# Optimization experiments

Hardware: AMD Instinct MI355X
Metric: run time of the kernel (lower is better)

## Reference

```python
import jax, jax.numpy as jnp
import numpy as np

NUM_EXPERTS = 8
CAPACITY = 320  # per-batch per-expert token capacity


def setup_inputs() -> dict:
    key = jax.random.key(0)
    k0, k1, k2, k3 = jax.random.split(key, 4)
    B, S, D, F = 4, 2048, 1024, 4096
    E = NUM_EXPERTS
    hidden_states = jax.random.normal(k0, (B, S, D), dtype=jnp.float32)
    gate_w = jax.random.normal(k1, (E, D), dtype=jnp.float32) * 0.02
    w1 = jax.random.normal(k2, (E, D, F), dtype=jnp.float32) * 0.02
    w2 = jax.random.normal(k3, (E, F, D), dtype=jnp.float32) * 0.02
    return {"hidden_states": hidden_states, "gate_w": gate_w, "w1": w1, "w2": w2}


def reference(hidden_states, gate_w, w1, w2):
    E, C = NUM_EXPERTS, CAPACITY
    B, S, D = hidden_states.shape

    # --- route ---
    router_logits = jnp.einsum('bsd,ed->bse', hidden_states, gate_w)
    router_probs = jax.nn.softmax(router_logits, axis=-1)
    expert_idx = jnp.argmax(router_probs, axis=-1)                      # [B,S]
    onehot = jax.nn.one_hot(expert_idx, E, dtype=jnp.int32)             # [B,S,E]
    priority = jnp.cumsum(onehot, axis=1)                               # [B,S,E]
    router_mask = onehot * (priority <= C)                              # [B,S,E]
    assigned = jnp.sum(router_mask, axis=-1) > 0                        # [B,S]
    # slot within expert buffer; dropped tokens go to overflow slot C
    slot = jnp.where(assigned, jnp.sum(priority * onehot, axis=-1) - 1, C)  # [B,S]
    top_prob = jnp.max(router_probs, axis=-1, keepdims=True)            # [B,S,1]

    # --- dispatch: scatter tokens into [B,E,C+1,D] buffers ---
    def dispatch(x_b, e_b, s_b):
        return jnp.zeros((E, C + 1, D), x_b.dtype).at[e_b, s_b].set(x_b)
    buf = jax.vmap(dispatch)(hidden_states, expert_idx, slot)           # [B,E,C+1,D]

    # --- per-expert FFN as grouped GEMM ---
    h = jax.nn.silu(jnp.einsum('becd,edf->becf', buf, w1))
    y = jnp.einsum('becf,efd->becd', h, w2)                             # [B,E,C+1,D]

    # --- combine: gather expert outputs back to token order ---
    gathered = jax.vmap(lambda y_b, e_b, s_b: y_b[e_b, s_b])(y, expert_idx, slot)  # [B,S,D]
    next_states = jnp.where(assigned[..., None], gathered, hidden_states)
    out = top_prob * next_states

    # argmax of capacity-masked one-hot: dropped tokens -> expert 0
    expert_index = jnp.where(assigned, expert_idx, 0)
    return out, router_logits, expert_index
```

## Files before the change

### kernel.cpp

```cpp
#include <hip/hip_runtime.h>

#define B_  4
#define S_  2048
#define D_  1024
#define F_  4096
#define E_  8
#define C_  320
#define CP_ 384
#define NT_ (B_*S_)
#define G_  (B_*E_)

typedef short bf16x8 __attribute__((ext_vector_type(8)));
typedef float f32x4  __attribute__((ext_vector_type(4)));

using gptr_t = const __attribute__((address_space(1))) void*;
using lptr_t = __attribute__((address_space(3))) void*;

__device__ static inline void gll16(const void* g, void* l) {
    __builtin_amdgcn_global_load_lds((gptr_t)g, (lptr_t)l, 16, 0, 0);
}

__device__ static inline unsigned short f2b(float f) {
    unsigned int u = __float_as_uint(f);
    u += 0x7fffu + ((u >> 16) & 1u);
    return (unsigned short)(u >> 16);
}

__global__ __launch_bounds__(256) void k_convT(const float* __restrict__ in,
                                               unsigned short* __restrict__ out,
                                               int R, int Cc) {
    __shared__ unsigned short ld[64][66];
    int e = blockIdx.z;
    const float* src = in + (size_t)e * R * Cc;
    unsigned short* dst = out + (size_t)e * R * Cc;
    int c0 = blockIdx.x * 64, r0 = blockIdx.y * 64;
    int t = threadIdx.x;

    int rr = t >> 4;
    int cg = t & 15;
#pragma unroll
    for (int p = 0; p < 4; p++) {
        int row = p * 16 + rr;
        float4 v = *(const float4*)(src + (size_t)(r0 + row) * Cc + c0 + cg * 4);
        ld[cg * 4 + 0][row] = f2b(v.x);
        ld[cg * 4 + 1][row] = f2b(v.y);
        ld[cg * 4 + 2][row] = f2b(v.z);
        ld[cg * 4 + 3][row] = f2b(v.w);
    }
    __syncthreads();

    int cc = t >> 3;
    int rg = t & 7;
#pragma unroll
    for (int p = 0; p < 2; p++) {
        int col = p * 32 + cc;
        const unsigned* lp = (const unsigned*)&ld[col][rg * 8];
        uint4 w;
        w.x = lp[0]; w.y = lp[1]; w.z = lp[2]; w.w = lp[3];
        *(uint4*)(dst + (size_t)(c0 + col) * R + r0 + rg * 8) = w;
    }
}

__global__ __launch_bounds__(256) void k_router(const float* __restrict__ hs,
                                                const float* __restrict__ gw,
                                                float* __restrict__ logits,
                                                int* __restrict__ eidx,
                                                float* __restrict__ tp) {
    int tok  = (int)((blockIdx.x * 256 + threadIdx.x) >> 6);
    int lane = threadIdx.x & 63;
    const float* x = hs + (size_t)tok * D_;
    double acc[E_];
#pragma unroll
    for (int e = 0; e < E_; e++) acc[e] = 0.0;
    for (int i = 0; i < 16; i++) {
        float xv = x[lane + 64 * i];
#pragma unroll
        for (int e = 0; e < E_; e++)
            acc[e] += (double)xv * (double)gw[e * D_ + lane + 64 * i];
    }
#pragma unroll
    for (int e = 0; e < E_; e++) {
#pragma unroll
        for (int off = 32; off > 0; off >>= 1)
            acc[e] += __shfl_xor(acc[e], off, 64);
    }
    if (lane == 0) {
        float l[E_];
        float mx = -1e30f; int am = 0;
#pragma unroll
        for (int e = 0; e < E_; e++) {
            l[e] = (float)acc[e];
            if (l[e] > mx) { mx = l[e]; am = e; }
        }
        float se = 0.f;
#pragma unroll
        for (int e = 0; e < E_; e++) se += __expf(l[e] - mx);
        tp[tok]   = 1.0f / se;
        eidx[tok] = am;
#pragma unroll
        for (int e = 0; e < E_; e++) logits[(size_t)tok * E_ + e] = l[e];
    }
}

__global__ __launch_bounds__(256) void k_scan(const int* __restrict__ eidx,
                                              int* __restrict__ slot,
                                              int* __restrict__ tok_list,
                                              int* __restrict__ counts,
                                              float* __restrict__ eif) {
    int b = blockIdx.x;
    __shared__ int cCnt[32][E_];
    __shared__ int cBase[32][E_];
    int t = threadIdx.x, wv = t >> 6, lane = t & 63;
    const int* eb = eidx + b * S_;
    for (int c = wv; c < 32; c += 4) {
        int e = eb[c * 64 + lane];
#pragma unroll
        for (int x = 0; x < E_; x++) {
            unsigned long long m = __ballot(e == x);
            if (lane == 0) cCnt[c][x] = __popcll(m);
        }
    }
    __syncthreads();
    if (t < E_) {
        int s = 0;
        for (int c = 0; c < 32; c++) { cBase[c][t] = s; s += cCnt[c][t]; }
        counts[b * E_ + t] = s;
    }
    __syncthreads();
    for (int c = wv; c < 32; c += 4) {
        int s_tok = c * 64 + lane;
        int e = eb[s_tok];
        unsigned long long lowmask = (1ull << lane) - 1ull;
        int rank = 0;
#pragma unroll
        for (int x = 0; x < E_; x++) {
            unsigned long long m = __ballot(e == x);
            if (x == e) rank = __popcll(m & lowmask);
        }
        int pos = cBase[c][e] + rank;
        int assigned = (pos < C_);
        slot[b * S_ + s_tok] = assigned ? pos : C_;
        if (assigned) tok_list[(b * E_ + e) * C_ + pos] = s_tok;
        eif[b * S_ + s_tok] = assigned ? (float)e : 0.0f;
    }
}

__global__ __launch_bounds__(256) void k_dispatch(const float* __restrict__ hs,
                                                  const int* __restrict__ tok_list,
                                                  const int* __restrict__ counts,
                                                  unsigned short* __restrict__ Xd) {
    int w    = (int)((blockIdx.x * 256 + threadIdx.x) >> 6);
    int lane = threadIdx.x & 63;
    int g = w / CP_, row = w % CP_;
    int b = g >> 3;
    int n = min(counts[g], C_);
    unsigned short* drow = Xd + ((size_t)g * CP_ + row) * D_;
    if (row < n) {
        int ts = tok_list[g * C_ + row];
        const float* src = hs + ((size_t)b * S_ + ts) * D_;
#pragma unroll
        for (int i = 0; i < 2; i++) {
            int c0 = (lane + 64 * i) * 8;
            float4 v0 = *(const float4*)(src + c0);
            float4 v1 = *(const float4*)(src + c0 + 4);
            uint4 pk;
            pk.x = (unsigned)f2b(v0.x) | ((unsigned)f2b(v0.y) << 16);
            pk.y = (unsigned)f2b(v0.z) | ((unsigned)f2b(v0.w) << 16);
            pk.z = (unsigned)f2b(v1.x) | ((unsigned)f2b(v1.y) << 16);
            pk.w = (unsigned)f2b(v1.z) | ((unsigned)f2b(v1.w) << 16);
            *(uint4*)(drow + c0) = pk;
        }
    } else {
        uint4 z = {0u, 0u, 0u, 0u};
#pragma unroll
        for (int i = 0; i < 2; i++)
            *(uint4*)(drow + (lane + 64 * i) * 8) = z;
    }
}

__global__ __launch_bounds__(256) void k_ffn1(const unsigned short* __restrict__ Xd,
                                              const unsigned short* __restrict__ w1t,
                                              const int* __restrict__ counts,
                                              unsigned short* __restrict__ h) {
    int zz = blockIdx.z;
    int g = (zz & 3) * 8 + (zz >> 2);
    int n_tok = min(counts[g], C_);
    int m0 = blockIdx.y * 128;
    if (m0 >= n_tok) return;
    int n0 = blockIdx.x * 128;
    int e = g & 7;

    __shared__ unsigned short As[128 * 32];
    __shared__ unsigned short Bs[128 * 32];
    int t = threadIdx.x, lane = t & 63, wv = t >> 6, wm = wv >> 1, wn = wv & 1;

    const unsigned short* Ap = Xd  + (size_t)g * CP_ * D_ + (size_t)(m0 + (t >> 2)) * D_ + (t & 3) * 8;
    const unsigned short* Bp = w1t + (size_t)e * F_ * D_  + (size_t)(n0 + (t >> 2)) * D_ + (t & 3) * 8;

    f32x4 acc[4][4];
    f32x4 z = {0.f, 0.f, 0.f, 0.f};
#pragma unroll
    for (int i = 0; i < 4; i++)
#pragma unroll
        for (int j = 0; j < 4; j++) acc[i][j] = z;

    int ar = (wm * 64 + (lane & 15)) * 32 + (lane >> 4) * 8;
    int br = (wn * 64 + (lane & 15)) * 32 + (lane >> 4) * 8;

    for (int kt = 0; kt < D_; kt += 32) {
        __syncthreads();
        gll16(Ap,            (char*)As + wv * 1024);
        gll16(Ap + 64 * D_,  (char*)As + 4096 + wv * 1024);
        gll16(Bp,            (char*)Bs + wv * 1024);
        gll16(Bp + 64 * D_,  (char*)Bs + 4096 + wv * 1024);
        Ap += 32; Bp += 32;
        __syncthreads();
        bf16x8 a[4], bq[4];
#pragma unroll
        for (int i = 0; i < 4; i++) a[i]  = *(const bf16x8*)&As[ar + i * 512];
#pragma unroll
        for (int j = 0; j < 4; j++) bq[j] = *(const bf16x8*)&Bs[br + j * 512];
#pragma unroll
        for (int i = 0; i < 4; i++)
#pragma unroll
            for (int j = 0; j < 4; j++)
                acc[i][j] = __builtin_amdgcn_mfma_f32_16x16x32_bf16(a[i], bq[j], acc[i][j], 0, 0, 0);
    }

    unsigned short* hb = h + (size_t)g * CP_ * F_;
    int crow = m0 + wm * 64 + (lane >> 4) * 4;
    int ccol = n0 + wn * 64 + (lane & 15);
#pragma unroll
    for (int i = 0; i < 4; i++)
#pragma unroll
        for (int r = 0; r < 4; r++) {
            int row = crow + i * 16 + r;
#pragma unroll
            for (int j = 0; j < 4; j++) {
                float v = acc[i][j][r];
                v = v / (1.0f + __expf(-v));
                hb[(size_t)row * F_ + ccol + j * 16] = f2b(v);
            }
        }
}

__global__ __launch_bounds__(256) void k_ffn2(const unsigned short* __restrict__ h,
                                              const unsigned short* __restrict__ w2t,
                                              const int* __restrict__ counts,
                                              const int* __restrict__ tok_list,
                                              const float* __restrict__ tp,
                                              float* __restrict__ out) {
    int zz = blockIdx.z;
    int g = (zz & 3) * 8 + (zz >> 2);
    int n_tok = min(counts[g], C_);
    int m0 = blockIdx.y * 128;
    if (m0 >= n_tok) return;
    int n0 = blockIdx.x * 128;
    int b = g >> 3, e = g & 7;

    __shared__ unsigned short As[128 * 32];
    __shared__ unsigned short Bs[128 * 32];
    int t = threadIdx.x, lane = t & 63, wv = t >> 6, wm = wv >> 1, wn = wv & 1;

    const unsigned short* Ap = h   + (size_t)g * CP_ * F_ + (size_t)(m0 + (t >> 2)) * F_ + (t & 3) * 8;
    const unsigned short* Bp = w2t + (size_t)e * D_ * F_  + (size_t)(n0 + (t >> 2)) * F_ + (t & 3) * 8;

    f32x4 acc[4][4];
    f32x4 z = {0.f, 0.f, 0.f, 0.f};
#pragma unroll
    for (int i = 0; i < 4; i++)
#pragma unroll
        for (int j = 0; j < 4; j++) acc[i][j] = z;

    int ar = (wm * 64 + (lane & 15)) * 32 + (lane >> 4) * 8;
    int br = (wn * 64 + (lane & 15)) * 32 + (lane >> 4) * 8;

    for (int kt = 0; kt < F_; kt += 32) {
        __syncthreads();
        gll16(Ap,            (char*)As + wv * 1024);
        gll16(Ap + 64 * F_,  (char*)As + 4096 + wv * 1024);
        gll16(Bp,            (char*)Bs + wv * 1024);
        gll16(Bp + 64 * F_,  (char*)Bs + 4096 + wv * 1024);
        Ap += 32; Bp += 32;
        __syncthreads();
        bf16x8 a[4], bq[4];
#pragma unroll
        for (int i = 0; i < 4; i++) a[i]  = *(const bf16x8*)&As[ar + i * 512];
#pragma unroll
        for (int j = 0; j < 4; j++) bq[j] = *(const bf16x8*)&Bs[br + j * 512];
#pragma unroll
        for (int i = 0; i < 4; i++)
#pragma unroll
            for (int j = 0; j < 4; j++)
                acc[i][j] = __builtin_amdgcn_mfma_f32_16x16x32_bf16(a[i], bq[j], acc[i][j], 0, 0, 0);
    }

    int crow = m0 + wm * 64 + (lane >> 4) * 4;
    int ccol = n0 + wn * 64 + (lane & 15);
#pragma unroll
    for (int i = 0; i < 4; i++)
#pragma unroll
        for (int r = 0; r < 4; r++) {
            int row = crow + i * 16 + r;
            if (row < n_tok) {
                int ts = tok_list[g * C_ + row];
                float sc = tp[b * S_ + ts];
                float* orow = out + ((size_t)b * S_ + ts) * D_ + ccol;
#pragma unroll
                for (int j = 0; j < 4; j++)
                    orow[j * 16] = sc * acc[i][j][r];
            }
        }
}

__global__ __launch_bounds__(256) void k_pass(const float* __restrict__ hs,
                                              const int* __restrict__ slot,
                                              const float* __restrict__ tp,
                                              float* __restrict__ out) {
    int tok  = (int)((blockIdx.x * 256 + threadIdx.x) >> 6);
    int lane = threadIdx.x & 63;
    if (slot[tok] < C_) return;
    float sc = tp[tok];
    const float* src = hs + (size_t)tok * D_;
    float* dst = out + (size_t)tok * D_;
#pragma unroll
    for (int i = 0; i < 4; i++) {
        float4 v = *(const float4*)(src + (lane + 64 * i) * 4);
        v.x *= sc; v.y *= sc; v.z *= sc; v.w *= sc;
        *(float4*)(dst + (lane + 64 * i) * 4) = v;
    }
}

extern "C" void kernel_launch(void* const* d_in, const int* in_sizes, int n_in,
                              void* d_out, int out_size, void* d_ws, size_t ws_size,
                              hipStream_t stream) {
    const float* hs = (const float*)d_in[0];
    const float* gw = (const float*)d_in[1];
    const float* w1 = (const float*)d_in[2];
    const float* w2 = (const float*)d_in[3];

    float* out    = (float*)d_out;
    float* logits = out + (size_t)NT_ * D_;
    float* eif    = logits + (size_t)NT_ * E_;

    char* ws = (char*)d_ws;
    int*            eidx     = (int*)(ws + 0);
    int*            slot     = (int*)(ws + 65536);
    float*          tp       = (float*)(ws + 131072);
    int*            tok_list = (int*)(ws + 196608);
    int*            counts   = (int*)(ws + 262144);
    unsigned short* Xd       = (unsigned short*)(ws + 327680);
    unsigned short* w1t      = (unsigned short*)(ws + 33554432ull);
    unsigned short* w2t      = (unsigned short*)(ws + 100663296ull);
    unsigned short* hbuf     = (unsigned short*)(ws + 167772160ull);

    dim3 blk(256);
    k_convT<<<dim3(F_ / 64, D_ / 64, E_), blk, 0, stream>>>(w1, w1t, D_, F_);
    k_convT<<<dim3(D_ / 64, F_ / 64, E_), blk, 0, stream>>>(w2, w2t, F_, D_);
    k_router<<<dim3(NT_ / 4), blk, 0, stream>>>(hs, gw, logits, eidx, tp);
    k_scan<<<dim3(B_), blk, 0, stream>>>(eidx, slot, tok_list, counts, eif);
    k_dispatch<<<dim3(G_ * CP_ / 4), blk, 0, stream>>>(hs, tok_list, counts, Xd);
    k_ffn1<<<dim3(F_ / 128, CP_ / 128, G_), blk, 0, stream>>>(Xd, w1t, counts, hbuf);
    k_ffn2<<<dim3(D_ / 128, CP_ / 128, G_), blk, 0, stream>>>(hbuf, w2t, counts, tok_list, tp, out);
    k_pass<<<dim3(NT_ / 4), blk, 0, stream>>>(hs, slot, tp, out);
}
```

Before: 599.4 us.

## Merge batches per expert into one grouped GEMM with 256x256 double-buffered tiles

Tokens are now regrouped per expert across all batches into one padded M dimension, using new base offsets and a global token list. Each expert's weights are then streamed once per M-tile rather than once per batch-expert group. The FFN GEMMs use a shared core: 512 threads, 256x256 output tiles, double-buffered LDS filled by direct global-to-LDS loads, an XOR swizzle, and barrier-separated MFMA phases with priority boosts. This adds a small extra launch and uses 128KB of LDS per block. The second GEMM launches only 160 blocks, which may leave CUs idle.

```diff
diff --git a/kernel.cpp b/kernel.cpp
--- a/kernel.cpp
+++ b/kernel.cpp
@@ -6,9 +6,8 @@
 #define F_  4096
 #define E_  8
 #define C_  320
-#define CP_ 384
+#define MPAD_ 1280
 #define NT_ (B_*S_)
-#define G_  (B_*E_)
 
 typedef short bf16x8 __attribute__((ext_vector_type(8)));
 typedef float f32x4  __attribute__((ext_vector_type(4)));
@@ -145,18 +144,38 @@
     }
 }
 
+__global__ void k_base(const int* __restrict__ counts,
+                       int* __restrict__ ebase,
+                       int* __restrict__ nE) {
+    int e = threadIdx.x;
+    if (e < E_) {
+        int s = 0;
+#pragma unroll
+        for (int b = 0; b < B_; b++) {
+            ebase[b * E_ + e] = s;
+            s += min(counts[b * E_ + e], C_);
+        }
+        nE[e] = s;
+    }
+}
+
 __global__ __launch_bounds__(256) void k_dispatch(const float* __restrict__ hs,
-                                                  const int* __restrict__ tok_list,
-                                                  const int* __restrict__ counts,
+                                                  const int* __restrict__ tlB,
+                                                  const int* __restrict__ ebase,
+                                                  const int* __restrict__ nE,
+                                                  int* __restrict__ tlG,
                                                   unsigned short* __restrict__ Xd) {
     int w    = (int)((blockIdx.x * 256 + threadIdx.x) >> 6);
     int lane = threadIdx.x & 63;
-    int g = w / CP_, row = w % CP_;
-    int b = g >> 3;
-    int n = min(counts[g], C_);
-    unsigned short* drow = Xd + ((size_t)g * CP_ + row) * D_;
-    if (row < n) {
-        int ts = tok_list[g * C_ + row];
+    int e = w / MPAD_, r = w - e * MPAD_;
+    unsigned short* drow = Xd + ((size_t)e * MPAD_ + r) * D_;
+    if (r < nE[e]) {
+        int b = 0;
+#pragma unroll
+        for (int bb = 1; bb < B_; bb++) if (r >= ebase[bb * E_ + e]) b = bb;
+        int pos = r - ebase[b * E_ + e];
+        int ts  = tlB[(b * E_ + e) * C_ + pos];
+        if (lane == 0) tlG[e * MPAD_ + r] = b * S_ + ts;
         const float* src = hs + ((size_t)b * S_ + ts) * D_;
 #pragma unroll
         for (int i = 0; i < 2; i++) {
@@ -171,141 +190,221 @@
             *(uint4*)(drow + c0) = pk;
         }
     } else {
-        uint4 z = {0u, 0u, 0u, 0u};
+        uint4 zz = {0u, 0u, 0u, 0u};
 #pragma unroll
         for (int i = 0; i < 2; i++)
-            *(uint4*)(drow + (lane + 64 * i) * 8) = z;
-    }
-}
-
-__global__ __launch_bounds__(256) void k_ffn1(const unsigned short* __restrict__ Xd,
-                                              const unsigned short* __restrict__ w1t,
-                                              const int* __restrict__ counts,
-                                              unsigned short* __restrict__ h) {
-    int zz = blockIdx.z;
-    int g = (zz & 3) * 8 + (zz >> 2);
-    int n_tok = min(counts[g], C_);
-    int m0 = blockIdx.y * 128;
-    if (m0 >= n_tok) return;
-    int n0 = blockIdx.x * 128;
-    int e = g & 7;
-
-    __shared__ unsigned short As[128 * 32];
-    __shared__ unsigned short Bs[128 * 32];
-    int t = threadIdx.x, lane = t & 63, wv = t >> 6, wm = wv >> 1, wn = wv & 1;
-
-    const unsigned short* Ap = Xd  + (size_t)g * CP_ * D_ + (size_t)(m0 + (t >> 2)) * D_ + (t & 3) * 8;
-    const unsigned short* Bp = w1t + (size_t)e * F_ * D_  + (size_t)(n0 + (t >> 2)) * D_ + (t & 3) * 8;
-
-    f32x4 acc[4][4];
+            *(uint4*)(drow + (lane + 64 * i) * 8) = zz;
+    }
+}
+
+template<int LDK, int KT>
+__device__ __forceinline__ void gemm_core(const unsigned short* __restrict__ Ab,
+                                          const unsigned short* __restrict__ Bb,
+                                          char* sm, f32x4 (&acc)[8][4]) {
+    const int t    = threadIdx.x;
+    const int lane = t & 63;
+    const int wv   = t >> 6;
+    const int wm   = wv >> 2;
+    const int wn   = wv & 3;
+
+    const int sr = t >> 3;
+    const int scs = (t & 7) ^ (sr & 7);
+    const unsigned short* aS = Ab + (size_t)sr * LDK + scs * 8;
+    const unsigned short* bS = Bb + (size_t)sr * LDK + scs * 8;
+    char* ldsA = sm;
+    char* ldsB = sm + 65536;
+    const int sd = wv * 1024;
+
+    const int rl  = lane & 15;
+    const int sw  = lane & 7;
+    const int kg  = lane >> 4;
+    const int sx0 = ((kg    ) ^ sw) << 4;
+    const int sx1 = ((kg + 4) ^ sw) << 4;
+    const int aro = (wm * 128 + rl) * 128;
+    const int bro = (wn * 64  + rl) * 128;
+
+#pragma unroll
+    for (int j = 0; j < 4; j++) {
+        gll16(aS + (size_t)(j * 64) * LDK, ldsA + j * 8192 + sd);
+        gll16(bS + (size_t)(j * 64) * LDK, ldsB + j * 8192 + sd);
+    }
+    asm volatile("s_waitcnt vmcnt(0)" ::: "memory");
+    __builtin_amdgcn_sched_barrier(0);
+    __builtin_amdgcn_s_barrier();
+    __builtin_amdgcn_sched_barrier(0);
+
+#pragma unroll 1
+    for (int kt = 0; kt < KT; ++kt) {
+        const char* cA = ldsA + (kt & 1) * 32768;
+        const char* cB = ldsB + (kt & 1) * 32768;
+        bf16x8 av[4], bv[4];
+
+#pragma unroll
+        for (int j = 0; j < 4; j++) bv[j] = *(const bf16x8*)(cB + bro + j * 2048 + sx0);
+#pragma unroll
+        for (int i = 0; i < 4; i++) av[i] = *(const bf16x8*)(cA + aro + i * 2048 + sx0);
+        if (kt + 1 < KT) {
+            char* nA = ldsA + ((kt + 1) & 1) * 32768;
+            char* nB = ldsB + ((kt + 1) & 1) * 32768;
+            const unsigned short* aP = aS + (kt + 1) * 64;
+            const unsigned short* bP = bS + (kt + 1) * 64;
+#pragma unroll
+            for (int j = 0; j < 4; j++) {
+                gll16(aP + (size_t)(j * 64) * LDK, nA + j * 8192 + sd);
+                gll16(bP + (size_t)(j * 64) * LDK, nB + j * 8192 + sd);
+            }
+        }
+        __builtin_amdgcn_sched_barrier(0);
+        __builtin_amdgcn_s_barrier();
+        __builtin_amdgcn_sched_barrier(0);
+        __builtin_amdgcn_s_setprio(1);
+#pragma unroll
+        for (int i = 0; i < 4; i++)
+#pragma unroll
+            for (int j = 0; j < 4; j++)
+                acc[i][j] = __builtin_amdgcn_mfma_f32_16x16x32_bf16(av[i], bv[j], acc[i][j], 0, 0, 0);
+        __builtin_amdgcn_s_setprio(0);
+        __builtin_amdgcn_sched_barrier(0);
+        __builtin_amdgcn_s_barrier();
+        __builtin_amdgcn_sched_barrier(0);
+
+#pragma unroll
+        for (int i = 0; i < 4; i++) av[i] = *(const bf16x8*)(cA + aro + 8192 + i * 2048 + sx0);
+        __builtin_amdgcn_sched_barrier(0);
+        __builtin_amdgcn_s_barrier();
+        __builtin_amdgcn_sched_barrier(0);
+        __builtin_amdgcn_s_setprio(1);
+#pragma unroll
+        for (int i = 0; i < 4; i++)
+#pragma unroll
+            for (int j = 0; j < 4; j++)
+                acc[4 + i][j] = __builtin_amdgcn_mfma_f32_16x16x32_bf16(av[i], bv[j], acc[4 + i][j], 0, 0, 0);
+        __builtin_amdgcn_s_setprio(0);
+        __builtin_amdgcn_sched_barrier(0);
+        __builtin_amdgcn_s_barrier();
+        __builtin_amdgcn_sched_barrier(0);
+
+#pragma unroll
+        for (int j = 0; j < 4; j++) bv[j] = *(const bf16x8*)(cB + bro + j * 2048 + sx1);
+#pragma unroll
+        for (int i = 0; i < 4; i++) av[i] = *(const bf16x8*)(cA + aro + i * 2048 + sx1);
+        __builtin_amdgcn_sched_barrier(0);
+        __builtin_amdgcn_s_barrier();
+        __builtin_amdgcn_sched_barrier(0);
+        __builtin_amdgcn_s_setprio(1);
+#pragma unroll
+        for (int i = 0; i < 4; i++)
+#pragma unroll
+            for (int j = 0; j < 4; j++)
+                acc[i][j] = __builtin_amdgcn_mfma_f32_16x16x32_bf16(av[i], bv[j], acc[i][j], 0, 0, 0);
+        __builtin_amdgcn_s_setprio(0);
+        __builtin_amdgcn_sched_barrier(0);
+        __builtin_amdgcn_s_barrier();
+        __builtin_amdgcn_sched_barrier(0);
+
+#pragma unroll
+        for (int i = 0; i < 4; i++) av[i] = *(const bf16x8*)(cA + aro + 8192 + i * 2048 + sx1);
+        __builtin_amdgcn_sched_barrier(0);
+        __builtin_amdgcn_s_barrier();
+        __builtin_amdgcn_sched_barrier(0);
+        __builtin_amdgcn_s_setprio(1);
+#pragma unroll
+        for (int i = 0; i < 4; i++)
+#pragma unroll
+            for (int j = 0; j < 4; j++)
+                acc[4 + i][j] = __builtin_amdgcn_mfma_f32_16x16x32_bf16(av[i], bv[j], acc[4 + i][j], 0, 0, 0);
+        __builtin_amdgcn_s_setprio(0);
+        asm volatile("s_waitcnt vmcnt(0)" ::: "memory");
+        __builtin_amdgcn_sched_barrier(0);
+        __builtin_amdgcn_s_barrier();
+        __builtin_amdgcn_sched_barrier(0);
+    }
+}
+
+__global__ __launch_bounds__(512, 2) void k_ffn1(const unsigned short* __restrict__ Xd,
+                                                 const unsigned short* __restrict__ w1t,
+                                                 const int* __restrict__ nE,
+                                                 unsigned short* __restrict__ h) {
+    __shared__ __align__(16) char sm[131072];
+    int id  = blockIdx.x;
+    int e   = id & 7;
+    int rem = id >> 3;
+    int mt  = rem % 5;
+    int nt  = rem / 5;
+    int m0  = mt * 256;
+    if (m0 >= nE[e]) return;
+    int n0  = nt * 256;
+
+    f32x4 acc[8][4];
     f32x4 z = {0.f, 0.f, 0.f, 0.f};
 #pragma unroll
-    for (int i = 0; i < 4; i++)
+    for (int i = 0; i < 8; i++)
 #pragma unroll
         for (int j = 0; j < 4; j++) acc[i][j] = z;
 
-    int ar = (wm * 64 + (lane & 15)) * 32 + (lane >> 4) * 8;
-    int br = (wn * 64 + (lane & 15)) * 32 + (lane >> 4) * 8;
-
-    for (int kt = 0; kt < D_; kt += 32) {
-        __syncthreads();
-        gll16(Ap,            (char*)As + wv * 1024);
-        gll16(Ap + 64 * D_,  (char*)As + 4096 + wv * 1024);
-        gll16(Bp,            (char*)Bs + wv * 1024);
-        gll16(Bp + 64 * D_,  (char*)Bs + 4096 + wv * 1024);
-        Ap += 32; Bp += 32;
-        __syncthreads();
-        bf16x8 a[4], bq[4];
-#pragma unroll
-        for (int i = 0; i < 4; i++) a[i]  = *(const bf16x8*)&As[ar + i * 512];
-#pragma unroll
-        for (int j = 0; j < 4; j++) bq[j] = *(const bf16x8*)&Bs[br + j * 512];
-#pragma unroll
-        for (int i = 0; i < 4; i++)
-#pragma unroll
-            for (int j = 0; j < 4; j++)
-                acc[i][j] = __builtin_amdgcn_mfma_f32_16x16x32_bf16(a[i], bq[j], acc[i][j], 0, 0, 0);
-    }
-
-    unsigned short* hb = h + (size_t)g * CP_ * F_;
-    int crow = m0 + wm * 64 + (lane >> 4) * 4;
-    int ccol = n0 + wn * 64 + (lane & 15);
-#pragma unroll
-    for (int i = 0; i < 4; i++)
+    const unsigned short* Ab = Xd  + ((size_t)e * MPAD_ + m0) * D_;
+    const unsigned short* Bb = w1t + ((size_t)e * F_    + n0) * D_;
+    gemm_core<D_, D_ / 64>(Ab, Bb, sm, acc);
+
+    int lane = threadIdx.x & 63, wv = threadIdx.x >> 6, wm = wv >> 2, wn = wv & 3;
+    unsigned short* hb = h + (size_t)e * MPAD_ * F_;
+    int rb = m0 + wm * 128 + ((lane >> 4) << 2);
+    int cb = n0 + wn * 64 + (lane & 15);
+#pragma unroll
+    for (int i = 0; i < 8; i++)
 #pragma unroll
         for (int r = 0; r < 4; r++) {
-            int row = crow + i * 16 + r;
+            unsigned short* hr = hb + (size_t)(rb + i * 16 + r) * F_ + cb;
 #pragma unroll
             for (int j = 0; j < 4; j++) {
                 float v = acc[i][j][r];
                 v = v / (1.0f + __expf(-v));
-                hb[(size_t)row * F_ + ccol + j * 16] = f2b(v);
+                hr[j * 16] = f2b(v);
             }
         }
 }
 
-__global__ __launch_bounds__(256) void k_ffn2(const unsigned short* __restrict__ h,
-                                              const unsigned short* __restrict__ w2t,
-                                              const int* __restrict__ counts,
-                                              const int* __restrict__ tok_list,
-                                              const float* __restrict__ tp,
-                                              float* __restrict__ out) {
-    int zz = blockIdx.z;
-    int g = (zz & 3) * 8 + (zz >> 2);
-    int n_tok = min(counts[g], C_);
-    int m0 = blockIdx.y * 128;
-    if (m0 >= n_tok) return;
-    int n0 = blockIdx.x * 128;
-    int b = g >> 3, e = g & 7;
-
-    __shared__ unsigned short As[128 * 32];
-    __shared__ unsigned short Bs[128 * 32];
-    int t = threadIdx.x, lane = t & 63, wv = t >> 6, wm = wv >> 1, wn = wv & 1;
-
-    const unsigned short* Ap = h   + (size_t)g * CP_ * F_ + (size_t)(m0 + (t >> 2)) * F_ + (t & 3) * 8;
-    const unsigned short* Bp = w2t + (size_t)e * D_ * F_  + (size_t)(n0 + (t >> 2)) * F_ + (t & 3) * 8;
-
-    f32x4 acc[4][4];
+__global__ __launch_bounds__(512, 2) void k_ffn2(const unsigned short* __restrict__ h,
+                                                 const unsigned short* __restrict__ w2t,
+                                                 const int* __restrict__ nE,
+                                                 const int* __restrict__ tlG,
+                                                 const float* __restrict__ tp,
+                                                 float* __restrict__ out) {
+    __shared__ __align__(16) char sm[131072];
+    int id  = blockIdx.x;
+    int e   = id & 7;
+    int rem = id >> 3;
+    int mt  = rem % 5;
+    int nt  = rem / 5;
+    int m0  = mt * 256;
+    int n   = nE[e];
+    if (m0 >= n) return;
+    int n0  = nt * 256;
+
+    f32x4 acc[8][4];
     f32x4 z = {0.f, 0.f, 0.f, 0.f};
 #pragma unroll
-    for (int i = 0; i < 4; i++)
+    for (int i = 0; i < 8; i++)
 #pragma unroll
         for (int j = 0; j < 4; j++) acc[i][j] = z;
 
-    int ar = (wm * 64 + (lane & 15)) * 32 + (lane >> 4) * 8;
-    int br = (wn * 64 + (lane & 15)) * 32 + (lane >> 4) * 8;
-
-    for (int kt = 0; kt < F_; kt += 32) {
-        __syncthreads();
-        gll16(Ap,            (char*)As + wv * 1024);
-        gll16(Ap + 64 * F_,  (char*)As + 4096 + wv * 1024);
-        gll16(Bp,            (char*)Bs + wv * 1024);
-        gll16(Bp + 64 * F_,  (char*)Bs + 4096 + wv * 1024);
-        Ap += 32; Bp += 32;
-        __syncthreads();
-        bf16x8 a[4], bq[4];
-#pragma unroll
-        for (int i = 0; i < 4; i++) a[i]  = *(const bf16x8*)&As[ar + i * 512];
-#pragma unroll
-        for (int j = 0; j < 4; j++) bq[j] = *(const bf16x8*)&Bs[br + j * 512];
-#pragma unroll
-        for (int i = 0; i < 4; i++)
-#pragma unroll
-            for (int j = 0; j < 4; j++)
-                acc[i][j] = __builtin_amdgcn_mfma_f32_16x16x32_bf16(a[i], bq[j], acc[i][j], 0, 0, 0);
-    }
-
-    int crow = m0 + wm * 64 + (lane >> 4) * 4;
-    int ccol = n0 + wn * 64 + (lane & 15);
-#pragma unroll
-    for (int i = 0; i < 4; i++)
+    const unsigned short* Ab = h   + ((size_t)e * MPAD_ + m0) * F_;
+    const unsigned short* Bb = w2t + ((size_t)e * D_    + n0) * F_;
+    gemm_core<F_, F_ / 64>(Ab, Bb, sm, acc);
+
+    int lane = threadIdx.x & 63, wv = threadIdx.x >> 6, wm = wv >> 2, wn = wv & 3;
+    const int* tl = tlG + e * MPAD_;
+    int rb = m0 + wm * 128 + ((lane >> 4) << 2);
+    int cb = n0 + wn * 64 + (lane & 15);
+#pragma unroll
+    for (int i = 0; i < 8; i++)
 #pragma unroll
         for (int r = 0; r < 4; r++) {
-            int row = crow + i * 16 + r;
-            if (row < n_tok) {
-                int ts = tok_list[g * C_ + row];
-                float sc = tp[b * S_ + ts];
-                float* orow = out + ((size_t)b * S_ + ts) * D_ + ccol;
+            int row = rb + i * 16 + r;
+            if (row < n) {
+                int gt = tl[row];
+                float sc = tp[gt];
+                float* orow = out + (size_t)gt * D_ + cb;
 #pragma unroll
                 for (int j = 0; j < 4; j++)
                     orow[j * 16] = sc * acc[i][j][r];
@@ -344,23 +443,27 @@
     float* eif    = logits + (size_t)NT_ * E_;
 
     char* ws = (char*)d_ws;
-    int*            eidx     = (int*)(ws + 0);
-    int*            slot     = (int*)(ws + 65536);
-    float*          tp       = (float*)(ws + 131072);
-    int*            tok_list = (int*)(ws + 196608);
-    int*            counts   = (int*)(ws + 262144);
-    unsigned short* Xd       = (unsigned short*)(ws + 327680);
-    unsigned short* w1t      = (unsigned short*)(ws + 33554432ull);
-    unsigned short* w2t      = (unsigned short*)(ws + 100663296ull);
-    unsigned short* hbuf     = (unsigned short*)(ws + 167772160ull);
+    int*            eidx   = (int*)(ws + 0);
+    int*            slot   = (int*)(ws + 65536);
+    float*          tp     = (float*)(ws + 131072);
+    int*            tlB    = (int*)(ws + 196608);
+    int*            tlG    = (int*)(ws + 237568);
+    int*            counts = (int*)(ws + 278528);
+    int*            ebase  = (int*)(ws + 278784);
+    int*            nE     = (int*)(ws + 279040);
+    unsigned short* Xd     = (unsigned short*)(ws + 327680);
+    unsigned short* w1t    = (unsigned short*)(ws + 33554432ull);
+    unsigned short* w2t    = (unsigned short*)(ws + 100663296ull);
+    unsigned short* hbuf   = (unsigned short*)(ws + 167772160ull);
 
     dim3 blk(256);
     k_convT<<<dim3(F_ / 64, D_ / 64, E_), blk, 0, stream>>>(w1, w1t, D_, F_);
     k_convT<<<dim3(D_ / 64, F_ / 64, E_), blk, 0, stream>>>(w2, w2t, F_, D_);
     k_router<<<dim3(NT_ / 4), blk, 0, stream>>>(hs, gw, logits, eidx, tp);
-    k_scan<<<dim3(B_), blk, 0, stream>>>(eidx, slot, tok_list, counts, eif);
-    k_dispatch<<<dim3(G_ * CP_ / 4), blk, 0, stream>>>(hs, tok_list, counts, Xd);
-    k_ffn1<<<dim3(F_ / 128, CP_ / 128, G_), blk, 0, stream>>>(Xd, w1t, counts, hbuf);
-    k_ffn2<<<dim3(D_ / 128, CP_ / 128, G_), blk, 0, stream>>>(hbuf, w2t, counts, tok_list, tp, out);
+    k_scan<<<dim3(B_), blk, 0, stream>>>(eidx, slot, tlB, counts, eif);
+    k_base<<<dim3(1), dim3(64), 0, stream>>>(counts, ebase, nE);
+    k_dispatch<<<dim3(E_ * MPAD_ / 4), blk, 0, stream>>>(hs, tlB, ebase, nE, tlG, Xd);
+    k_ffn1<<<dim3(640), dim3(512), 0, stream>>>(Xd, w1t, nE, hbuf);
+    k_ffn2<<<dim3(160), dim3(512), 0, stream>>>(hbuf, w2t, nE, tlG, tp, out);
     k_pass<<<dim3(NT_ / 4), blk, 0, stream>>>(hs, slot, tp, out);
 }
```

Result: no change. 610.3 us (+1.8%).
